# Kernel optimization log

Hardware: AMD Instinct MI355X
Metric: run time of the kernel (lower is better)

Reference implementation:

```python
import jax, jax.numpy as jnp
import numpy as np

N_FFT = 512
HOP = 128
WIN = 512
LENGTH = 600  # hardcoded in the original forward


def _hann(n):
    # torch.hann_window default is periodic: 0.5*(1-cos(2*pi*i/n))
    i = jnp.arange(n, dtype=jnp.float32)
    return 0.5 * (1.0 - jnp.cos(2.0 * jnp.pi * i / n))


def setup_inputs() -> dict:
    key = jax.random.key(0)
    x = jax.random.normal(key, (8192, 1, 257, 6, 2), dtype=jnp.float32)
    return {"x": x}


def reference(x):
    B, C, F, T, D = x.shape  # C==1, F==n_fft//2+1, D==2
    # view(B, F, T, D) + view_as_complex
    spec = x[:, 0, :, :, 0] + 1j * x[:, 0, :, :, 1]          # [B, F, T] complex64
    # inverse real FFT per frame (torch.istft, normalized=False, onesided=True)
    frames = jnp.fft.irfft(spec.transpose(0, 2, 1), n=N_FFT, axis=-1)  # [B, T, n_fft]
    win = _hann(WIN)                                          # [n_fft] (win_length == n_fft)
    frames = frames * win                                     # synthesis windowing
    # overlap-add
    L = HOP * (T - 1) + N_FFT
    idx = jnp.arange(T)[:, None] * HOP + jnp.arange(N_FFT)[None, :]  # [T, n_fft]
    y = jnp.zeros((B, L), dtype=frames.dtype).at[:, idx].add(frames)  # [B, L]
    # window-square envelope normalization (COLA division)
    env = jnp.zeros((L,), dtype=frames.dtype).at[idx].add(win * win)  # [L]
    # center=True trim of n_fft//2, then length=600 crop
    start = N_FFT // 2
    sig = y[:, start:start + LENGTH] / env[start:start + LENGTH]       # [B, 600]
    return sig[:, None, :]                                    # unsqueeze(1) -> [B, 1, 600]
```

## Files before the change

kernel.cpp:

```cpp
#include <hip/hip_runtime.h>
#include <hip/hip_bf16.h>


#define NFFT   512
#define HOP    128
#define KDIM   3084
#define KP     3136
#define NOUT   600
#define NP     640
#define BM     64
#define BN     128

#define NFRAG_K 98
#define FRAG_SH 512
#define WTOT    ((size_t)(NP / 16) * NFRAG_K * FRAG_SH)

typedef short s16x8 __attribute__((ext_vector_type(8)));
typedef float f32x4 __attribute__((ext_vector_type(4)));

static __device__ __forceinline__ unsigned short bf16_bits(float f) {
    __hip_bfloat16 b = __float2bfloat16(f);
    return *(unsigned short*)&b;
}

static __device__ __forceinline__ s16x8 cvt_frag(float4 lo, float4 hi) {
    s16x8 r;
    r[0] = (short)bf16_bits(lo.x); r[1] = (short)bf16_bits(lo.y);
    r[2] = (short)bf16_bits(lo.z); r[3] = (short)bf16_bits(lo.w);
    r[4] = (short)bf16_bits(hi.x); r[5] = (short)bf16_bits(hi.y);
    r[6] = (short)bf16_bits(hi.z); r[7] = (short)bf16_bits(hi.w);
    return r;
}

__global__ __launch_bounds__(256) void gen_W(unsigned short* __restrict__ Wt,
                                             float4* __restrict__ outZ,
                                             int nvec4) {
    __shared__ float costab[512];
    __shared__ __align__(16) unsigned short rowbuf[KP];
    const int l   = blockIdx.x;
    const int tid = threadIdx.x;
    const float w0 = 6.283185307179586f / 512.0f;

    for (int i = blockIdx.x * 256 + tid; i < nvec4; i += NP * 256)
        outZ[i] = make_float4(0.f, 0.f, 0.f, 0.f);

    *(int4*)(rowbuf + tid * 8) = make_int4(0, 0, 0, 0);
    if (tid < 136) *(int4*)(rowbuf + (256 + tid) * 8) = make_int4(0, 0, 0, 0);
    costab[tid]       = __cosf((float)tid * w0);
    costab[tid + 256] = __cosf((float)(tid + 256) * w0);
    __syncthreads();

    if (l < NOUT) {
        const int p = l + 256;
        float env = 0.0f;
#pragma unroll
        for (int tt = 0; tt < 6; ++tt) {
            int m = p - HOP * tt;
            if (m >= 0 && m < NFFT) {
                float w = 0.5f - 0.5f * costab[m];
                env += w * w;
            }
        }
        const float inv = 1.0f / (512.0f * env);
        for (int f = tid; f <= 256; f += 256) {
            float cf = (f == 0 || f == 256) ? 1.0f : 2.0f;
#pragma unroll
            for (int t = 0; t < 6; ++t) {
                int n = p - HOP * t;
                if (n >= 0 && n < NFFT) {
                    float w = 0.5f - 0.5f * costab[n];
                    float scale = cf * w * inv;
                    int a = (f * n) & 511;
                    float c = costab[a];
                    float s = costab[(a + 384) & 511];
                    rowbuf[f * 12 + t * 2 + 0] = bf16_bits(scale * c);
                    rowbuf[f * 12 + t * 2 + 1] = bf16_bits(-scale * s);
                }
            }
        }
    }
    __syncthreads();

    const int n16 = l >> 4, r = l & 15;
    for (int u = tid; u < 392; u += 256) {
        const int kc = u >> 2, q = u & 3;
        int4 val = *(const int4*)(rowbuf + kc * 32 + q * 8);
        *(int4*)(Wt + (((size_t)n16 * NFRAG_K + kc) * 64 + q * 16 + r) * 8) = val;
    }
}

__global__ __launch_bounds__(256, 4) void gemm_kernel(
        const float* __restrict__ X,
        const unsigned short* __restrict__ Wt,
        float* __restrict__ out) {
    const int tid = threadIdx.x;
    const int bid  = blockIdx.x;
    const int xcd  = bid & 7;
    const int rest = bid >> 3;
    const int mt   = xcd * 16 + rest / 10;
    const int sub  = rest % 10;
    const int nt   = sub >> 1;
    const int kidx = sub & 1;
    const int mBase = mt * BM;
    const int nBase = nt * BN;

    const int lane = tid & 63;
    const int wave = tid >> 6;
    const int wm   = (wave & 1) * 32;
    const int wn   = (wave >> 1) * 64;
    const int lrow = lane & 15;
    const int quad = lane >> 4;

    const float* aRow0 = X + (size_t)(mBase + wm + lrow) * KDIM;
    const float* aRow1 = aRow0 + (size_t)16 * KDIM;
    const int kq = quad * 8;

    const int n16base = nt * 8 + (wave >> 1) * 4;
    const unsigned short* wB0 = Wt + (size_t)n16base * NFRAG_K * FRAG_SH
                                   + (size_t)lane * 8;

    f32x4 acc[2][4];
#pragma unroll
    for (int i = 0; i < 2; ++i)
#pragma unroll
        for (int j = 0; j < 4; ++j) acc[i][j] = (f32x4){0.f, 0.f, 0.f, 0.f};

#define LOADA(L0, H0, L1, H1, kc_)                                             \
    {                                                                          \
        const int kb_ = (kc_) * 32 + kq;                                       \
        L0 = *(const float4*)(aRow0 + kb_);                                    \
        H0 = *(const float4*)(aRow0 + kb_ + 4);                                \
        L1 = *(const float4*)(aRow1 + kb_);                                    \
        H1 = *(const float4*)(aRow1 + kb_ + 4);                                \
    }

#define LOADB(BV, kc_)                                                         \
    {                                                                          \
        _Pragma("unroll")                                                      \
        for (int j = 0; j < 4; ++j)                                            \
            BV[j] = *(const s16x8*)(const void*)(wB0 +                         \
                        ((size_t)j * NFRAG_K + (size_t)(kc_)) * FRAG_SH);      \
    }

#define COMPUTE(L0, H0, L1, H1, BV)                                            \
    {                                                                          \
        s16x8 af0 = cvt_frag(L0, H0);                                          \
        s16x8 af1 = cvt_frag(L1, H1);                                          \
        _Pragma("unroll")                                                      \
        for (int j = 0; j < 4; ++j)                                            \
            acc[0][j] = __builtin_amdgcn_mfma_f32_16x16x32_bf16(               \
                af0, BV[j], acc[0][j], 0, 0, 0);                               \
        _Pragma("unroll")                                                      \
        for (int j = 0; j < 4; ++j)                                            \
            acc[1][j] = __builtin_amdgcn_mfma_f32_16x16x32_bf16(               \
                af1, BV[j], acc[1][j], 0, 0, 0);                               \
    }

    const int kcBeg = kidx ? 50 : 0;
    const int kcEnd = kidx ? 96 : 50;

    float4 a0l0, a0h0, a1l0, a1h0;
    float4 a0l1, a0h1, a1l1, a1h1;
    s16x8  bv0[4], bv1[4];

    LOADA(a0l0, a0h0, a1l0, a1h0, kcBeg);
    LOADB(bv0, kcBeg);
    for (int kc = kcBeg; kc + 1 < kcEnd; kc += 2) {
        LOADA(a0l1, a0h1, a1l1, a1h1, kc + 1);
        LOADB(bv1, kc + 1);
        COMPUTE(a0l0, a0h0, a1l0, a1h0, bv0);
        if (kc + 2 < kcEnd) {
            LOADA(a0l0, a0h0, a1l0, a1h0, kc + 2);
            LOADB(bv0, kc + 2);
        }
        COMPUTE(a0l1, a0h1, a1l1, a1h1, bv1);
    }

    if (kidx) {
        const int kb = 96 * 32 + kq;
        float e0[8], e1[8];
#pragma unroll
        for (int e = 0; e < 8; ++e) {
            const int k = kb + e;
            const bool ok = (k < KDIM);
            e0[e] = ok ? aRow0[k] : 0.f;
            e1[e] = ok ? aRow1[k] : 0.f;
        }
        float4 l0 = make_float4(e0[0], e0[1], e0[2], e0[3]);
        float4 h0 = make_float4(e0[4], e0[5], e0[6], e0[7]);
        float4 l1 = make_float4(e1[0], e1[1], e1[2], e1[3]);
        float4 h1 = make_float4(e1[4], e1[5], e1[6], e1[7]);
        LOADB(bv0, 96);
        COMPUTE(l0, h0, l1, h1, bv0);
    }

#undef LOADA
#undef LOADB
#undef COMPUTE

#pragma unroll
    for (int i = 0; i < 2; ++i) {
#pragma unroll
        for (int j = 0; j < 4; ++j) {
            int gn = nBase + wn + j * 16 + lrow;
            if (gn < NOUT) {
#pragma unroll
                for (int r = 0; r < 4; ++r) {
                    int gm = mBase + wm + i * 16 + quad * 4 + r;
                    atomicAdd(out + (size_t)gm * NOUT + gn, acc[i][j][r]);
                }
            }
        }
    }
}

extern "C" void kernel_launch(void* const* d_in, const int* in_sizes, int n_in,
                              void* d_out, int out_size, void* d_ws, size_t ws_size,
                              hipStream_t stream) {
    const float* X = (const float*)d_in[0];
    unsigned short* W = (unsigned short*)d_ws;
    float* out = (float*)d_out;

    gen_W<<<dim3(NP), 256, 0, stream>>>(W, (float4*)d_out, out_size / 4);
    gemm_kernel<<<dim3(128 * 5 * 2), 256, 0, stream>>>(X, W, out);
}
```

Before: 284.8 us.

## Stage A tiles through LDS with async global_load_lds double buffering

The fp32 input rows are no longer loaded straight into registers per wave. Each block now DMAs 64x64 float tiles into XOR-swizzled LDS with global_load_lds and double-buffers them across 24 tiles per K half. Waves then read their fragments from LDS, which is meant to give coalesced global reads and overlap the loads with MFMA work. The cost is a block-wide barrier on every tile and 32KB of LDS per block, which may reduce occupancy. The K split also moves from 50/46 to 48/48 chunks.

```diff
diff --git a/kernel.cpp b/kernel.cpp
--- a/kernel.cpp
+++ b/kernel.cpp
@@ -10,10 +10,12 @@
 #define NP     640
 #define BM     64
 #define BN     128
+#define NTILES 24
 
 #define NFRAG_K 98
 #define FRAG_SH 512
 #define WTOT    ((size_t)(NP / 16) * NFRAG_K * FRAG_SH)
+#define GRIDB   (128 * 5 * 2)
 
 typedef short s16x8 __attribute__((ext_vector_type(8)));
 typedef float f32x4 __attribute__((ext_vector_type(4)));
@@ -30,6 +32,12 @@
     r[4] = (short)bf16_bits(hi.x); r[5] = (short)bf16_bits(hi.y);
     r[6] = (short)bf16_bits(hi.z); r[7] = (short)bf16_bits(hi.w);
     return r;
+}
+
+static __device__ __forceinline__ void gload_lds16(const void* g, void* l) {
+    __builtin_amdgcn_global_load_lds(
+        (const __attribute__((address_space(1))) unsigned int*)g,
+        (__attribute__((address_space(3))) unsigned int*)l, 16, 0, 0);
 }
 
 __global__ __launch_bounds__(256) void gen_W(unsigned short* __restrict__ Wt,
@@ -93,6 +101,8 @@
         const float* __restrict__ X,
         const unsigned short* __restrict__ Wt,
         float* __restrict__ out) {
+    __shared__ __align__(16) float As[2][4096];
+
     const int tid = threadIdx.x;
     const int bid  = blockIdx.x;
     const int xcd  = bid & 7;
@@ -103,6 +113,7 @@
     const int kidx = sub & 1;
     const int mBase = mt * BM;
     const int nBase = nt * BN;
+    const int gBeg  = kidx * NTILES;
 
     const int lane = tid & 63;
     const int wave = tid >> 6;
@@ -111,29 +122,25 @@
     const int lrow = lane & 15;
     const int quad = lane >> 4;
 
-    const float* aRow0 = X + (size_t)(mBase + wm + lrow) * KDIM;
-    const float* aRow1 = aRow0 + (size_t)16 * KDIM;
-    const int kq = quad * 8;
+    const int rQ  = wave * 4 + (lane >> 4);
+    const int sLg = (lane & 15) ^ (rQ & 7);
+    const float* dmaSrc = X + (size_t)(mBase + rQ) * KDIM + sLg * 4;
+    char* ldsB0 = (char*)&As[0][0];
+    char* ldsB1 = (char*)&As[1][0];
+
+#define DMA_TILE(LB, g_)                                                       \
+    {                                                                          \
+        const float* s_ = dmaSrc + (size_t)(g_) * 64;                          \
+        _Pragma("unroll")                                                      \
+        for (int u = 0; u < 4; ++u)                                            \
+            gload_lds16(s_ + (size_t)u * 16 * KDIM,                            \
+                        (LB) + u * 4096 + wave * 1024);                        \
+    }
 
     const int n16base = nt * 8 + (wave >> 1) * 4;
     const unsigned short* wB0 = Wt + (size_t)n16base * NFRAG_K * FRAG_SH
                                    + (size_t)lane * 8;
 
-    f32x4 acc[2][4];
-#pragma unroll
-    for (int i = 0; i < 2; ++i)
-#pragma unroll
-        for (int j = 0; j < 4; ++j) acc[i][j] = (f32x4){0.f, 0.f, 0.f, 0.f};
-
-#define LOADA(L0, H0, L1, H1, kc_)                                             \
-    {                                                                          \
-        const int kb_ = (kc_) * 32 + kq;                                       \
-        L0 = *(const float4*)(aRow0 + kb_);                                    \
-        H0 = *(const float4*)(aRow0 + kb_ + 4);                                \
-        L1 = *(const float4*)(aRow1 + kb_);                                    \
-        H1 = *(const float4*)(aRow1 + kb_ + 4);                                \
-    }
-
 #define LOADB(BV, kc_)                                                         \
     {                                                                          \
         _Pragma("unroll")                                                      \
@@ -142,10 +149,27 @@
                         ((size_t)j * NFRAG_K + (size_t)(kc_)) * FRAG_SH);      \
     }
 
-#define COMPUTE(L0, H0, L1, H1, BV)                                            \
-    {                                                                          \
-        s16x8 af0 = cvt_frag(L0, H0);                                          \
-        s16x8 af1 = cvt_frag(L1, H1);                                          \
+    f32x4 acc[2][4];
+#pragma unroll
+    for (int i = 0; i < 2; ++i)
+#pragma unroll
+        for (int j = 0; j < 4; ++j) acc[i][j] = (f32x4){0.f, 0.f, 0.f, 0.f};
+
+#define AFRAG(AF, LB, i16, ks)                                                 \
+    {                                                                          \
+        const int R_  = wm + (i16) * 16 + lrow;                                \
+        const int sp_ = (ks) * 8 + quad * 2;                                   \
+        const int x_  = R_ & 7;                                                \
+        float4 f0_ = *(const float4*)((LB) + R_ * 256 + ((sp_)     ^ x_) * 16);\
+        float4 f1_ = *(const float4*)((LB) + R_ * 256 + ((sp_ + 1) ^ x_) * 16);\
+        AF = cvt_frag(f0_, f1_);                                               \
+    }
+
+#define COMPUTE_KS(LB, ks, BV)                                                 \
+    {                                                                          \
+        s16x8 af0, af1;                                                        \
+        AFRAG(af0, LB, 0, ks);                                                 \
+        AFRAG(af1, LB, 1, ks);                                                 \
         _Pragma("unroll")                                                      \
         for (int j = 0; j < 4; ++j)                                            \
             acc[0][j] = __builtin_amdgcn_mfma_f32_16x16x32_bf16(               \
@@ -156,28 +180,28 @@
                 af1, BV[j], acc[1][j], 0, 0, 0);                               \
     }
 
-    const int kcBeg = kidx ? 50 : 0;
-    const int kcEnd = kidx ? 96 : 50;
-
-    float4 a0l0, a0h0, a1l0, a1h0;
-    float4 a0l1, a0h1, a1l1, a1h1;
-    s16x8  bv0[4], bv1[4];
-
-    LOADA(a0l0, a0h0, a1l0, a1h0, kcBeg);
-    LOADB(bv0, kcBeg);
-    for (int kc = kcBeg; kc + 1 < kcEnd; kc += 2) {
-        LOADA(a0l1, a0h1, a1l1, a1h1, kc + 1);
-        LOADB(bv1, kc + 1);
-        COMPUTE(a0l0, a0h0, a1l0, a1h0, bv0);
-        if (kc + 2 < kcEnd) {
-            LOADA(a0l0, a0h0, a1l0, a1h0, kc + 2);
-            LOADB(bv0, kc + 2);
-        }
-        COMPUTE(a0l1, a0h1, a1l1, a1h1, bv1);
+    s16x8 bv0[4], bv1[4];
+    DMA_TILE(ldsB0, gBeg);
+    LOADB(bv0, 2 * gBeg);
+    LOADB(bv1, 2 * gBeg + 1);
+    __syncthreads();
+
+    for (int t = 0; t < NTILES; ++t) {
+        const int g = gBeg + t;
+        char* LB = (t & 1) ? ldsB1 : ldsB0;
+        char* LN = (t & 1) ? ldsB0 : ldsB1;
+        if (t + 1 < NTILES) DMA_TILE(LN, g + 1);
+        COMPUTE_KS(LB, 0, bv0);
+        if (t + 1 < NTILES) LOADB(bv0, 2 * (g + 1));
+        COMPUTE_KS(LB, 1, bv1);
+        if (t + 1 < NTILES) LOADB(bv1, 2 * (g + 1) + 1);
+        __syncthreads();
     }
 
     if (kidx) {
-        const int kb = 96 * 32 + kq;
+        const float* aRow0 = X + (size_t)(mBase + wm + lrow) * KDIM;
+        const float* aRow1 = aRow0 + (size_t)16 * KDIM;
+        const int kb = 96 * 32 + quad * 8;
         float e0[8], e1[8];
 #pragma unroll
         for (int e = 0; e < 8; ++e) {
@@ -191,12 +215,22 @@
         float4 l1 = make_float4(e1[0], e1[1], e1[2], e1[3]);
         float4 h1 = make_float4(e1[4], e1[5], e1[6], e1[7]);
         LOADB(bv0, 96);
-        COMPUTE(l0, h0, l1, h1, bv0);
-    }
-
-#undef LOADA
+        s16x8 af0 = cvt_frag(l0, h0);
+        s16x8 af1 = cvt_frag(l1, h1);
+#pragma unroll
+        for (int j = 0; j < 4; ++j)
+            acc[0][j] = __builtin_amdgcn_mfma_f32_16x16x32_bf16(
+                af0, bv0[j], acc[0][j], 0, 0, 0);
+#pragma unroll
+        for (int j = 0; j < 4; ++j)
+            acc[1][j] = __builtin_amdgcn_mfma_f32_16x16x32_bf16(
+                af1, bv0[j], acc[1][j], 0, 0, 0);
+    }
+
+#undef DMA_TILE
 #undef LOADB
-#undef COMPUTE
+#undef AFRAG
+#undef COMPUTE_KS
 
 #pragma unroll
     for (int i = 0; i < 2; ++i) {
@@ -222,5 +256,5 @@
     float* out = (float*)d_out;
 
     gen_W<<<dim3(NP), 256, 0, stream>>>(W, (float4*)d_out, out_size / 4);
-    gemm_kernel<<<dim3(128 * 5 * 2), 256, 0, stream>>>(X, W, out);
-}
+    gemm_kernel<<<dim3(GRIDB), 256, 0, stream>>>(X, W, out);
+}
```

After: 237.3 us. 1.2x faster.

## Stage A and B tiles through a 4-deep LDS ring via async global-to-LDS loads

Applied to the files above, without the earlier changes.

Replaces per-wave direct global loads of X rows and W fragments with global_load_lds DMA into a four-stage shared-memory ring buffer, using XOR swizzling for A rows and explicit vmcnt waits plus barriers. B fragments are now fetched once per block and shared across waves instead of being loaded redundantly by each wave. The K split is rebalanced to 48 steps per half. The 64 KB LDS footprint lowers the occupancy target from 4 to 2 blocks per CU, which reduces latency hiding from extra resident waves.

```diff
diff --git a/kernel.cpp b/kernel.cpp
--- a/kernel.cpp
+++ b/kernel.cpp
@@ -10,10 +10,12 @@
 #define NP     640
 #define BM     64
 #define BN     128
+#define NT     48
 
 #define NFRAG_K 98
 #define FRAG_SH 512
 #define WTOT    ((size_t)(NP / 16) * NFRAG_K * FRAG_SH)
+#define GRIDB   (128 * 5 * 2)
 
 typedef short s16x8 __attribute__((ext_vector_type(8)));
 typedef float f32x4 __attribute__((ext_vector_type(4)));
@@ -30,6 +32,12 @@
     r[4] = (short)bf16_bits(hi.x); r[5] = (short)bf16_bits(hi.y);
     r[6] = (short)bf16_bits(hi.z); r[7] = (short)bf16_bits(hi.w);
     return r;
+}
+
+static __device__ __forceinline__ void gload_lds16(const void* g, void* l) {
+    __builtin_amdgcn_global_load_lds(
+        (const __attribute__((address_space(1))) unsigned int*)g,
+        (__attribute__((address_space(3))) unsigned int*)l, 16, 0, 0);
 }
 
 __global__ __launch_bounds__(256) void gen_W(unsigned short* __restrict__ Wt,
@@ -89,10 +97,12 @@
     }
 }
 
-__global__ __launch_bounds__(256, 4) void gemm_kernel(
+__global__ __launch_bounds__(256, 2) void gemm_kernel(
         const float* __restrict__ X,
         const unsigned short* __restrict__ Wt,
         float* __restrict__ out) {
+    __shared__ __align__(16) unsigned char LDSc[4 * 16384];
+
     const int tid = threadIdx.x;
     const int bid  = blockIdx.x;
     const int xcd  = bid & 7;
@@ -103,81 +113,92 @@
     const int kidx = sub & 1;
     const int mBase = mt * BM;
     const int nBase = nt * BN;
+    const int sBeg  = kidx * NT;
 
     const int lane = tid & 63;
     const int wave = tid >> 6;
     const int wm   = (wave & 1) * 32;
-    const int wn   = (wave >> 1) * 64;
+    const int wn2  = (wave >> 1) * 64;
     const int lrow = lane & 15;
     const int quad = lane >> 4;
 
-    const float* aRow0 = X + (size_t)(mBase + wm + lrow) * KDIM;
-    const float* aRow1 = aRow0 + (size_t)16 * KDIM;
-    const int kq = quad * 8;
+    const int grow0 = (wave * 2 + 0) * 8 + (lane >> 3);
+    const int grow1 = (wave * 2 + 1) * 8 + (lane >> 3);
+    const float* aSrc0 = X + (size_t)(mBase + grow0) * KDIM
+                           + (((lane & 7) ^ (grow0 & 7)) * 4);
+    const float* aSrc1 = X + (size_t)(mBase + grow1) * KDIM
+                           + (((lane & 7) ^ (grow1 & 7)) * 4);
+
+    const unsigned short* bSrc0 = Wt + ((size_t)(nt * 8 + wave * 2 + 0)
+                                        * NFRAG_K) * FRAG_SH + (size_t)lane * 8;
+    const unsigned short* bSrc1 = Wt + ((size_t)(nt * 8 + wave * 2 + 1)
+                                        * NFRAG_K) * FRAG_SH + (size_t)lane * 8;
 
     const int n16base = nt * 8 + (wave >> 1) * 4;
     const unsigned short* wB0 = Wt + (size_t)n16base * NFRAG_K * FRAG_SH
                                    + (size_t)lane * 8;
 
+#define DMA_SET(set_, s_)                                                      \
+    {                                                                          \
+        char* aDst = (char*)LDSc + (set_) * 16384;                             \
+        char* bDst = aDst + 8192;                                              \
+        gload_lds16(aSrc0 + (size_t)(s_) * 32, aDst + (wave * 2 + 0) * 1024);  \
+        gload_lds16(aSrc1 + (size_t)(s_) * 32, aDst + (wave * 2 + 1) * 1024);  \
+        gload_lds16(bSrc0 + (size_t)(s_) * FRAG_SH,                            \
+                    bDst + (wave * 2 + 0) * 1024);                             \
+        gload_lds16(bSrc1 + (size_t)(s_) * FRAG_SH,                            \
+                    bDst + (wave * 2 + 1) * 1024);                             \
+    }
+
     f32x4 acc[2][4];
 #pragma unroll
     for (int i = 0; i < 2; ++i)
 #pragma unroll
         for (int j = 0; j < 4; ++j) acc[i][j] = (f32x4){0.f, 0.f, 0.f, 0.f};
 
-#define LOADA(L0, H0, L1, H1, kc_)                                             \
+#define COMPUTE_SET(set_)                                                      \
     {                                                                          \
-        const int kb_ = (kc_) * 32 + kq;                                       \
-        L0 = *(const float4*)(aRow0 + kb_);                                    \
-        H0 = *(const float4*)(aRow0 + kb_ + 4);                                \
-        L1 = *(const float4*)(aRow1 + kb_);                                    \
-        H1 = *(const float4*)(aRow1 + kb_ + 4);                                \
-    }
-
-#define LOADB(BV, kc_)                                                         \
-    {                                                                          \
+        const char* aB = (const char*)LDSc + (set_) * 16384;                   \
+        const char* bB = aB + 8192;                                            \
+        s16x8 bfr[4];                                                          \
         _Pragma("unroll")                                                      \
-        for (int j = 0; j < 4; ++j)                                            \
-            BV[j] = *(const s16x8*)(const void*)(wB0 +                         \
-                        ((size_t)j * NFRAG_K + (size_t)(kc_)) * FRAG_SH);      \
-    }
-
-#define COMPUTE(L0, H0, L1, H1, BV)                                            \
-    {                                                                          \
-        s16x8 af0 = cvt_frag(L0, H0);                                          \
-        s16x8 af1 = cvt_frag(L1, H1);                                          \
+        for (int jj = 0; jj < 4; ++jj)                                         \
+            bfr[jj] = *(const s16x8*)(const void*)(bB +                        \
+                          ((wave >> 1) * 4 + jj) * 1024 + lane * 16);          \
         _Pragma("unroll")                                                      \
-        for (int j = 0; j < 4; ++j)                                            \
-            acc[0][j] = __builtin_amdgcn_mfma_f32_16x16x32_bf16(               \
-                af0, BV[j], acc[0][j], 0, 0, 0);                               \
-        _Pragma("unroll")                                                      \
-        for (int j = 0; j < 4; ++j)                                            \
-            acc[1][j] = __builtin_amdgcn_mfma_f32_16x16x32_bf16(               \
-                af1, BV[j], acc[1][j], 0, 0, 0);                               \
-    }
-
-    const int kcBeg = kidx ? 50 : 0;
-    const int kcEnd = kidx ? 96 : 50;
-
-    float4 a0l0, a0h0, a1l0, a1h0;
-    float4 a0l1, a0h1, a1l1, a1h1;
-    s16x8  bv0[4], bv1[4];
-
-    LOADA(a0l0, a0h0, a1l0, a1h0, kcBeg);
-    LOADB(bv0, kcBeg);
-    for (int kc = kcBeg; kc + 1 < kcEnd; kc += 2) {
-        LOADA(a0l1, a0h1, a1l1, a1h1, kc + 1);
-        LOADB(bv1, kc + 1);
-        COMPUTE(a0l0, a0h0, a1l0, a1h0, bv0);
-        if (kc + 2 < kcEnd) {
-            LOADA(a0l0, a0h0, a1l0, a1h0, kc + 2);
-            LOADB(bv0, kc + 2);
-        }
-        COMPUTE(a0l1, a0h1, a1l1, a1h1, bv1);
+        for (int i = 0; i < 2; ++i) {                                          \
+            const int R_ = wm + i * 16 + lrow;                                 \
+            const int x_ = R_ & 7;                                             \
+            float4 f0_ = *(const float4*)(aB + R_ * 128 +                      \
+                             (((quad * 2) ^ x_) * 16));                        \
+            float4 f1_ = *(const float4*)(aB + R_ * 128 +                      \
+                             (((quad * 2 + 1) ^ x_) * 16));                    \
+            s16x8 af_ = cvt_frag(f0_, f1_);                                    \
+            _Pragma("unroll")                                                  \
+            for (int jj = 0; jj < 4; ++jj)                                     \
+                acc[i][jj] = __builtin_amdgcn_mfma_f32_16x16x32_bf16(          \
+                    af_, bfr[jj], acc[i][jj], 0, 0, 0);                        \
+        }                                                                      \
+    }
+
+    DMA_SET(0, sBeg + 0);
+    DMA_SET(1, sBeg + 1);
+    DMA_SET(2, sBeg + 2);
+
+    for (int t = 0; t < NT; ++t) {
+        if (t <= NT - 3)      asm volatile("s_waitcnt vmcnt(8) lgkmcnt(0)" ::: "memory");
+        else if (t == NT - 2) asm volatile("s_waitcnt vmcnt(4) lgkmcnt(0)" ::: "memory");
+        else                  asm volatile("s_waitcnt vmcnt(0) lgkmcnt(0)" ::: "memory");
+        __builtin_amdgcn_s_barrier();
+        __builtin_amdgcn_sched_barrier(0);
+        if (t + 3 < NT) DMA_SET((t + 3) & 3, sBeg + t + 3);
+        COMPUTE_SET(t & 3);
     }
 
     if (kidx) {
-        const int kb = 96 * 32 + kq;
+        const float* aRow0 = X + (size_t)(mBase + wm + lrow) * KDIM;
+        const float* aRow1 = aRow0 + (size_t)16 * KDIM;
+        const int kb = 96 * 32 + quad * 8;
         float e0[8], e1[8];
 #pragma unroll
         for (int e = 0; e < 8; ++e) {
@@ -190,19 +211,31 @@
         float4 h0 = make_float4(e0[4], e0[5], e0[6], e0[7]);
         float4 l1 = make_float4(e1[0], e1[1], e1[2], e1[3]);
         float4 h1 = make_float4(e1[4], e1[5], e1[6], e1[7]);
-        LOADB(bv0, 96);
-        COMPUTE(l0, h0, l1, h1, bv0);
-    }
-
-#undef LOADA
-#undef LOADB
-#undef COMPUTE
+        s16x8 bvt[4];
+#pragma unroll
+        for (int j = 0; j < 4; ++j)
+            bvt[j] = *(const s16x8*)(const void*)(wB0 +
+                         ((size_t)j * NFRAG_K + 96) * FRAG_SH);
+        s16x8 af0 = cvt_frag(l0, h0);
+        s16x8 af1 = cvt_frag(l1, h1);
+#pragma unroll
+        for (int j = 0; j < 4; ++j)
+            acc[0][j] = __builtin_amdgcn_mfma_f32_16x16x32_bf16(
+                af0, bvt[j], acc[0][j], 0, 0, 0);
+#pragma unroll
+        for (int j = 0; j < 4; ++j)
+            acc[1][j] = __builtin_amdgcn_mfma_f32_16x16x32_bf16(
+                af1, bvt[j], acc[1][j], 0, 0, 0);
+    }
+
+#undef DMA_SET
+#undef COMPUTE_SET
 
 #pragma unroll
     for (int i = 0; i < 2; ++i) {
 #pragma unroll
         for (int j = 0; j < 4; ++j) {
-            int gn = nBase + wn + j * 16 + lrow;
+            int gn = nBase + wn2 + j * 16 + lrow;
             if (gn < NOUT) {
 #pragma unroll
                 for (int r = 0; r < 4; ++r) {
@@ -222,5 +255,5 @@
     float* out = (float*)d_out;
 
     gen_W<<<dim3(NP), 256, 0, stream>>>(W, (float4*)d_out, out_size / 4);
-    gemm_kernel<<<dim3(128 * 5 * 2), 256, 0, stream>>>(X, W, out);
-}
+    gemm_kernel<<<dim3(GRIDB), 256, 0, stream>>>(X, W, out);
+}
```

After: 295.8 us. +3.8%, slower.
